# Optimization experiments

Hardware: AMD Instinct MI355X
Metric: run time of the kernel (lower is better)

Reference implementation:

```python
import jax, jax.numpy as jnp
import numpy as np
import math

N, H, D_MODEL = 2048, 16, 2048
D_K = D_MODEL // H
D_FF = 4 * D_MODEL
EPS = 1e-5


def _layernorm(x, alpha, beta):
    # torch: mean/var over dim=1 (=feature dim for 2D input), unbiased=False
    m = jnp.mean(x, axis=1, keepdims=True)
    v = jnp.var(x, axis=1, keepdims=True)
    return (x - m) / jnp.sqrt(v + EPS) * alpha + beta


def setup_inputs() -> dict:
    key = jax.random.key(0)
    ks = jax.random.split(key, 12)
    s = 0.02  # weight init scale
    return {
        "X": jax.random.normal(ks[0], (N, D_MODEL), jnp.float32),
        "Wq": jax.random.normal(ks[1], (H, D_MODEL, D_K), jnp.float32) * s,
        "bq": jax.random.normal(ks[2], (H, D_K), jnp.float32) * s,
        "Wk": jax.random.normal(ks[3], (H, D_MODEL, D_K), jnp.float32) * s,
        "bk": jax.random.normal(ks[4], (H, D_K), jnp.float32) * s,
        "Wv": jax.random.normal(ks[5], (H, D_MODEL, D_K), jnp.float32) * s,
        "bv": jax.random.normal(ks[6], (H, D_K), jnp.float32) * s,
        "alpha1": jnp.ones((N, D_MODEL), jnp.float32),
        "beta1": jnp.zeros((N, D_MODEL), jnp.float32),
        "W1": jax.random.normal(ks[7], (D_MODEL, D_FF), jnp.float32) * s,
        "b1": jax.random.normal(ks[8], (D_FF,), jnp.float32) * s,
        "W2": jax.random.normal(ks[9], (D_FF, D_MODEL), jnp.float32) * s,
        "b2": jax.random.normal(ks[10], (D_MODEL,), jnp.float32) * s,
        "alpha2": jnp.ones((N, D_MODEL), jnp.float32),
        "beta2": jnp.zeros((N, D_MODEL), jnp.float32),
    }


def reference(X, Wq, bq, Wk, bk, Wv, bv, alpha1, beta1, W1, b1, W2, b2, alpha2, beta2):
    # --- Multi-headed self-attention (h per-head linears fused as stacked weights) ---
    Q = jnp.einsum('nd,hdk->hnk', X, Wq) + bq[:, None, :]  # (H, N, D_K)
    K = jnp.einsum('nd,hdk->hnk', X, Wk) + bk[:, None, :]
    V = jnp.einsum('nd,hdk->hnk', X, Wv) + bv[:, None, :]
    scores = jnp.einsum('hnk,hmk->hnm', Q, K) / math.sqrt(D_K)  # (H, N, N)
    A = jax.nn.softmax(scores, axis=-1)  # softmax over keys (torch dim=1 of 2D)
    O = jnp.einsum('hnm,hmk->hnk', A, V)  # (H, N, D_K)
    attn = jnp.transpose(O, (1, 0, 2)).reshape(N, D_MODEL)  # concat heads on dim=1
    # --- Add & Norm 1 (dropout is identity at inference) ---
    h1 = _layernorm(X + attn, alpha1, beta1)
    # --- FFN ---
    ffn = jnp.maximum(h1 @ W1 + b1, 0.0) @ W2 + b2
    # --- Add & Norm 2 ---
    return _layernorm(h1 + ffn, alpha2, beta2)
```

## Files before the change

### kernel.cpp

```cpp
#include <hip/hip_runtime.h>
#include <hip/hip_bf16.h>

#define N_TOK 2048
#define DMODEL 2048
#define NH 16
#define DK 128
#define DFF 8192

typedef __attribute__((ext_vector_type(8))) short short8;
typedef __attribute__((ext_vector_type(4))) short s16x4;
typedef __attribute__((ext_vector_type(4))) float f32x4;

__device__ __forceinline__ short f2bf(float f) {
    unsigned int x = __builtin_bit_cast(unsigned int, f);
    unsigned int r = (x + 0x7fffu + ((x >> 16) & 1u)) >> 16;
    return (short)r;
}

__global__ __launch_bounds__(256) void cast_f32_bf16(const float* __restrict__ in,
                                                     short* __restrict__ out, int n8) {
    int i = blockIdx.x * 256 + threadIdx.x;
    if (i >= n8) return;
    const float4* p = (const float4*)in + (size_t)i * 2;
    float4 a = p[0], b = p[1];
    short8 o;
    o[0] = f2bf(a.x); o[1] = f2bf(a.y); o[2] = f2bf(a.z); o[3] = f2bf(a.w);
    o[4] = f2bf(b.x); o[5] = f2bf(b.y); o[6] = f2bf(b.z); o[7] = f2bf(b.w);
    *(short8*)(out + (size_t)i * 8) = o;
}

template <typename TIN>
__global__ __launch_bounds__(256) void transpose_cast(const TIN* __restrict__ in,
                                                      short* __restrict__ out,
                                                      int R, int C, long sIn, long sOut) {
    __shared__ float t[64][65];
    in  += (long)blockIdx.z * sIn;
    out += (long)blockIdx.z * sOut;
    int tx = threadIdx.x & 63, ty = threadIdx.x >> 6;
    long r0 = (long)blockIdx.y * 64, c0 = (long)blockIdx.x * 64;
    for (int i = 0; i < 16; i++) {
        int r = ty + i * 4;
        t[r][tx] = (float)in[(r0 + r) * (long)C + c0 + tx];
    }
    __syncthreads();
    for (int i = 0; i < 16; i++) {
        int r = ty + i * 4;
        out[(c0 + r) * (long)R + r0 + tx] = f2bf(t[tx][r]);
    }
}

__device__ __forceinline__ void gld_lds16(const void* g, void* l) {
    __builtin_amdgcn_global_load_lds(
        (const __attribute__((address_space(1))) void*)g,
        (__attribute__((address_space(3))) void*)l, 16, 0, 0);
}

#define VM8 asm volatile("s_waitcnt vmcnt(8)" ::: "memory")
#define VM0 asm volatile("s_waitcnt vmcnt(0)" ::: "memory")
#define VMNONE ((void)0)

#define PHASE(BUF, MH, NHI, RA, RBNH, STAGE_STMT, VMSTMT)                       \
  {                                                                             \
    if (RA) {                                                                   \
      _Pragma("unroll") for (int mp = 0; mp < 4; mp++)                          \
        _Pragma("unroll") for (int kk = 0; kk < 2; kk++) {                      \
          int rowA = wr * 128 + (MH) * 64 + mp * 16 + fr;                       \
          af[mp][kk] = *(const short8*)((const char*)lds + (BUF) * 65536 +      \
                         rowA * 128 + (((kk * 4 + fq) ^ (rowA & 7)) << 4));     \
        }                                                                       \
    }                                                                           \
    if ((RBNH) < 2) {                                                           \
      _Pragma("unroll") for (int np = 0; np < 2; np++)                          \
        _Pragma("unroll") for (int kk = 0; kk < 2; kk++) {                      \
          int rowB = wc * 64 + (RBNH) * 32 + np * 16 + fr;                      \
          bf[(RBNH) & 1][np][kk] =                                              \
              *(const short8*)((const char*)lds + (BUF) * 65536 + 32768 +       \
                  rowB * 128 + (((kk * 4 + fq) ^ (rowB & 7)) << 4));            \
        }                                                                       \
    }                                                                           \
    STAGE_STMT;                                                                 \
    __builtin_amdgcn_s_barrier();                                               \
    asm volatile("s_waitcnt lgkmcnt(0)" ::: "memory");                          \
    __builtin_amdgcn_sched_barrier(0);                                          \
    __builtin_amdgcn_s_setprio(1);                                              \
    _Pragma("unroll") for (int mp = 0; mp < 4; mp++)                            \
      _Pragma("unroll") for (int np = 0; np < 2; np++)                          \
        _Pragma("unroll") for (int kk = 0; kk < 2; kk++)                        \
          acc[(MH) * 4 + mp][(NHI) * 2 + np] =                                  \
              __builtin_amdgcn_mfma_f32_16x16x32_bf16(                          \
                  af[mp][kk], bf[NHI][np][kk], acc[(MH) * 4 + mp][(NHI) * 2 + np],\
                  0, 0, 0);                                                     \
    __builtin_amdgcn_s_setprio(0);                                              \
    VMSTMT;                                                                     \
    __builtin_amdgcn_sched_barrier(0);                                          \
    __builtin_amdgcn_s_barrier();                                               \
    __builtin_amdgcn_sched_barrier(0);                                          \
  }

template <int MODE>
__global__ __launch_bounds__(512, 2) void gemm256(const short* __restrict__ A,
                                                  const short* __restrict__ Bt,
                                                  void* __restrict__ Cv,
                                                  const float* __restrict__ b0,
                                                  const float* __restrict__ b1,
                                                  const float* __restrict__ b2,
                                                  int Ktot, int TM) {
    __shared__ short lds[65536];
    const int tid = threadIdx.x, lane = tid & 63, w = tid >> 6;
    const int T = gridDim.x, bid = blockIdx.x;
    const int vbid = (bid & 7) * (T >> 3) + (bid >> 3);
    const int mt = vbid % TM;
    const int rest = vbid / TM;
    int nt = rest, z = 0;
    if (MODE == 2) { nt = rest & 7; z = rest >> 3; }
    const long brow = (long)mt * 256, bcol = (long)nt * 256;
    const short* Ab = A + (MODE == 2 ? (long)z * 2048 : 0);
    const short* Bb = Bt + (MODE == 2 ? (long)z * 2048 : 0);

    auto stageA = [&](int kt, int buf, int mh) {
#pragma unroll
        for (int j = 0; j < 2; j++) {
            int row = mh * 64 + j * 128 + (tid >> 3);
            int g = (lane & 7) ^ (row & 7);
            gld_lds16((const char*)(Ab + (brow + row) * (long)Ktot + (long)kt * 64) + g * 16,
                      (char*)lds + buf * 65536 + mh * 8192 + j * 16384 + w * 1024 + lane * 16);
        }
    };
    auto stageB = [&](int kt, int buf, int nh) {
#pragma unroll
        for (int j = 0; j < 2; j++) {
            int s = 2 * j + (w >> 2);
            int rin = (w & 3) * 8 + (lane >> 3);
            int row = s * 64 + nh * 32 + rin;
            int g = (lane & 7) ^ (row & 7);
            gld_lds16((const char*)(Bb + (bcol + row) * (long)Ktot + (long)kt * 64) + g * 16,
                      (char*)lds + buf * 65536 + 32768 + j * 16384 + (w >> 2) * 8192 +
                          nh * 4096 + (w & 3) * 1024 + lane * 16);
        }
    };

    const int wr = w >> 2, wc = w & 3;
    const int fr = lane & 15, fq = lane >> 4;
    f32x4 acc[8][4] = {};
    short8 af[4][2], bf[2][2][2];

    stageA(0, 0, 0); stageB(0, 0, 0); stageB(0, 0, 1); stageA(0, 0, 1);
    stageA(1, 1, 0); stageB(1, 1, 0); stageB(1, 1, 1); stageA(1, 1, 1);
    VM8;
    __builtin_amdgcn_s_barrier();

    for (int i = 0; i < 15; i++) {
        const int kn = 2 * i + 2;
        PHASE(0, 0, 0, 1, 0, {}, VMNONE)
        PHASE(0, 0, 1, 0, 1, { stageA(kn, 0, 0); stageB(kn, 0, 0); }, VMNONE)
        PHASE(0, 1, 0, 1, 2, { stageB(kn, 0, 1); }, VMNONE)
        PHASE(0, 1, 1, 0, 2, { stageA(kn, 0, 1); }, VM8)
        PHASE(1, 0, 0, 1, 0, {}, VMNONE)
        PHASE(1, 0, 1, 0, 1, { stageA(kn + 1, 1, 0); stageB(kn + 1, 1, 0); }, VMNONE)
        PHASE(1, 1, 0, 1, 2, { stageB(kn + 1, 1, 1); }, VMNONE)
        PHASE(1, 1, 1, 0, 2, { stageA(kn + 1, 1, 1); }, VM8)
    }
    PHASE(0, 0, 0, 1, 0, {}, VMNONE)
    PHASE(0, 0, 1, 0, 1, {}, VMNONE)
    PHASE(0, 1, 0, 1, 2, {}, VMNONE)
    PHASE(0, 1, 1, 0, 2, {}, VM0)
    PHASE(1, 0, 0, 1, 0, {}, VMNONE)
    PHASE(1, 0, 1, 0, 1, {}, VMNONE)
    PHASE(1, 1, 0, 1, 2, {}, VMNONE)
    PHASE(1, 1, 1, 0, 2, {}, VMNONE)

    const long crow0 = brow + wr * 128, ccol0 = bcol + wc * 64;
#pragma unroll
    for (int n = 0; n < 4; n++) {
        const long col = ccol0 + (n >> 1) * 32 + (n & 1) * 16 + fr;
        float bval = 0.f;
        if (MODE == 0) {
            const float* bp = (col >> 11) == 0 ? b0 : (col >> 11) == 1 ? b1 : b2;
            bval = bp[col & 2047];
        } else if (MODE == 1) bval = b0[col];
#pragma unroll
        for (int m = 0; m < 8; m++) {
#pragma unroll
            for (int r = 0; r < 4; r++) {
                const long row = crow0 + (m >> 2) * 64 + (m & 3) * 16 + fq * 4 + r;
                float v = acc[m][n][r] + bval;
                if (MODE == 0) {
                    const long slab = col >> 7;
                    ((short*)Cv)[slab * (2048L * 128) + row * 128 + (col & 127)] = f2bf(v);
                } else if (MODE == 1) {
                    ((short*)Cv)[row * 8192 + col] = f2bf(fmaxf(v, 0.f));
                } else {
                    ((float*)Cv)[(long)z * (2048L * 2048) + row * 2048 + col] = v;
                }
            }
        }
    }
}

__global__ __launch_bounds__(512, 2) void attn_flash(const short* __restrict__ Q,
                                                     const short* __restrict__ Kc,
                                                     const short* __restrict__ VT,
                                                     float* __restrict__ O) {
    __shared__ short lds[32768];
    const int tid = threadIdx.x, lane = tid & 63, w = tid >> 6;
    const int bid = blockIdx.x;
    const int vid = (bid & 7) * 32 + (bid >> 3);
    const int h = vid >> 4, qt = vid & 15;
    const int fr = lane & 15, fq = lane >> 4;
    const long qbase = (long)qt * 128 + w * 16;
    const short* Qh = Q  + (long)h * N_TOK * DK;
    const short* Kh = Kc + (long)h * N_TOK * DK;
    const short* Vh = VT + (long)h * DK * N_TOK;
    short* Pw = lds + 24576 + w * 1024;

    short8 qf[4];
#pragma unroll
    for (int c = 0; c < 4; c++)
        qf[c] = *(const short8*)(Qh + (qbase + fr) * DK + c * 32 + fq * 8);

    float mrow = -1e30f, lrow = 0.f;
    f32x4 oacc[8] = {};
    const float C1 = 0.08838834764831845f * 1.4426950408889634f;

    int wr_off[4], rd_off[2];
#pragma unroll
    for (int jc = 0; jc < 4; jc++)
        wr_off[jc] = (fr * 64 + jc * 16 + fq * 4) ^ ((fr & 7) << 3);
#pragma unroll
    for (int kc = 0; kc < 2; kc++)
        rd_off[kc] = (fr * 64 + kc * 32 + fq * 8) ^ ((fr & 7) << 3);
    int colKb[4], colVb[2];
#pragma unroll
    for (int c = 0; c < 4; c++) colKb[c] = (c * 64 + fq * 16) ^ ((fr & 7) << 4);
#pragma unroll
    for (int kc = 0; kc < 2; kc++) colVb[kc] = (kc * 64 + fq * 16) ^ ((fr & 7) << 4);

    auto stageK = [&](int kvt, int buf) {
        const char* Kg = (const char*)(Kh + (long)kvt * 64 * DK);
        char* Kd = (char*)(lds + buf * 8192);
#pragma unroll
        for (int i = 0; i < 2; i++) {
            int a = (w * 2 + i) * 1024 + (lane << 4);
            int src = a ^ (((a >> 8) & 7) << 4);
            gld_lds16(Kg + src, Kd + (w * 2 + i) * 1024);
        }
    };
    auto stageV = [&](int kvt) {
        char* Vd = (char*)(lds + 16384);
#pragma unroll
        for (int i = 0; i < 2; i++) {
            int a = (w * 2 + i) * 1024 + (lane << 4);
            int row = a >> 7;
            int inner = (a & 127) ^ ((row & 7) << 4);
            const char* src = (const char*)Vh + ((long)row * N_TOK + (long)kvt * 64) * 2 + inner;
            gld_lds16(src, Vd + (w * 2 + i) * 1024);
        }
    };

    const int NT = N_TOK / 64;
    stageK(0, 0);
    __syncthreads();

    for (int t = 0; t < NT; t++) {
        const int cur = t & 1;
        stageV(t);
        if (t + 1 < NT) stageK(t + 1, cur ^ 1);

        const char* Kcb = (const char*)(lds + cur * 8192);
        f32x4 s[4] = {};
#pragma unroll
        for (int jc = 0; jc < 4; jc++) {
            const char* rb = Kcb + (jc * 16 + fr) * 256;
#pragma unroll
            for (int c = 0; c < 4; c++) {
                short8 kf = *(const short8*)(rb + colKb[c]);
                s[jc] = __builtin_amdgcn_mfma_f32_16x16x32_bf16(kf, qf[c], s[jc], 0, 0, 0);
            }
        }

        float tm = -1e30f;
#pragma unroll
        for (int jc = 0; jc < 4; jc++)
#pragma unroll
            for (int r = 0; r < 4; r++) tm = fmaxf(tm, s[jc][r]);
        tm = fmaxf(tm, __shfl_xor(tm, 16));
        tm = fmaxf(tm, __shfl_xor(tm, 32));
        float nm = fmaxf(mrow, tm);
        float resc = exp2f(C1 * (mrow - nm));
        mrow = nm;
        float sum = 0.f;
#pragma unroll
        for (int jc = 0; jc < 4; jc++)
#pragma unroll
            for (int r = 0; r < 4; r++) {
                float p = exp2f(C1 * (s[jc][r] - nm));
                s[jc][r] = p;
                sum += p;
            }
        sum += __shfl_xor(sum, 16);
        sum += __shfl_xor(sum, 32);
        lrow = lrow * resc + sum;
#pragma unroll
        for (int f = 0; f < 8; f++)
#pragma unroll
            for (int r = 0; r < 4; r++) oacc[f][r] *= resc;

#pragma unroll
        for (int jc = 0; jc < 4; jc++) {
            s16x4 pk;
            pk[0] = f2bf(s[jc][0]); pk[1] = f2bf(s[jc][1]);
            pk[2] = f2bf(s[jc][2]); pk[3] = f2bf(s[jc][3]);
            *(s16x4*)(Pw + wr_off[jc]) = pk;
        }
        short8 pa[2];
#pragma unroll
        for (int kc = 0; kc < 2; kc++)
            pa[kc] = *(const short8*)(Pw + rd_off[kc]);

        __syncthreads();

        const char* Vcb = (const char*)(lds + 16384);
#pragma unroll
        for (int f = 0; f < 8; f++) {
            const char* rb = Vcb + (f * 16 + fr) * 128;
#pragma unroll
            for (int kc = 0; kc < 2; kc++) {
                short8 vf = *(const short8*)(rb + colVb[kc]);
                oacc[f] = __builtin_amdgcn_mfma_f32_16x16x32_bf16(vf, pa[kc], oacc[f], 0, 0, 0);
            }
        }
        __syncthreads();
    }

    const float inv = 1.f / lrow;
    const long row = qbase + fr;
#pragma unroll
    for (int f = 0; f < 8; f++) {
        float4 o;
        o.x = oacc[f][0] * inv; o.y = oacc[f][1] * inv;
        o.z = oacc[f][2] * inv; o.w = oacc[f][3] * inv;
        *(float4*)(O + row * (long)DMODEL + h * DK + f * 16 + fq * 4) = o;
    }
}

template <bool WBF>
__global__ __launch_bounds__(256) void add_ln(const float* __restrict__ A,
                                              const float* __restrict__ B,
                                              const float* __restrict__ alpha,
                                              const float* __restrict__ beta,
                                              float* __restrict__ out,
                                              short* __restrict__ outbf) {
    const int row = blockIdx.x, t = threadIdx.x;
    const long base = (long)row * DMODEL;
    float4 va[2], vb[2];
    float s = 0.f, q = 0.f;
#pragma unroll
    for (int i = 0; i < 2; i++) {
        long off = base + (long)(t + i * 256) * 4;
        va[i] = *(const float4*)(A + off);
        vb[i] = *(const float4*)(B + off);
        float x0 = va[i].x + vb[i].x, x1 = va[i].y + vb[i].y;
        float x2 = va[i].z + vb[i].z, x3 = va[i].w + vb[i].w;
        s += x0 + x1 + x2 + x3;
        q += x0 * x0 + x1 * x1 + x2 * x2 + x3 * x3;
    }
#pragma unroll
    for (int o = 1; o < 64; o <<= 1) { s += __shfl_xor(s, o); q += __shfl_xor(q, o); }
    __shared__ float red[8];
    if ((t & 63) == 0) { red[t >> 6] = s; red[4 + (t >> 6)] = q; }
    __syncthreads();
    s = red[0] + red[1] + red[2] + red[3];
    q = red[4] + red[5] + red[6] + red[7];
    const float mean = s * (1.f / DMODEL);
    const float var = q * (1.f / DMODEL) - mean * mean;
    const float rstd = rsqrtf(var + 1e-5f);
#pragma unroll
    for (int i = 0; i < 2; i++) {
        long off = base + (long)(t + i * 256) * 4;
        float4 al = *(const float4*)(alpha + off);
        float4 be = *(const float4*)(beta + off);
        float x[4] = { va[i].x + vb[i].x, va[i].y + vb[i].y, va[i].z + vb[i].z, va[i].w + vb[i].w };
        float a[4] = { al.x, al.y, al.z, al.w };
        float b[4] = { be.x, be.y, be.z, be.w };
#pragma unroll
        for (int j = 0; j < 4; j++) {
            float o2 = (x[j] - mean) * rstd * a[j] + b[j];
            out[off + j] = o2;
            if (WBF) outbf[off + j] = f2bf(o2);
        }
    }
}

__global__ __launch_bounds__(256) void add_ln2_red(const float* __restrict__ H1,
                                                   const float* __restrict__ F4,
                                                   const float* __restrict__ b2,
                                                   const float* __restrict__ alpha,
                                                   const float* __restrict__ beta,
                                                   float* __restrict__ out) {
    const int row = blockIdx.x, t = threadIdx.x;
    const long base = (long)row * DMODEL;
    const long SL = (long)N_TOK * DMODEL;
    float x[8];
    float s = 0.f, q = 0.f;
#pragma unroll
    for (int i = 0; i < 2; i++) {
        long off = base + (long)(t + i * 256) * 4;
        int col = (t + i * 256) * 4;
        float4 a  = *(const float4*)(H1 + off);
        float4 f0 = *(const float4*)(F4 + off);
        float4 f1 = *(const float4*)(F4 + off + SL);
        float4 f2 = *(const float4*)(F4 + off + 2 * SL);
        float4 f3 = *(const float4*)(F4 + off + 3 * SL);
        float4 bb = *(const float4*)(b2 + col);
        x[i * 4 + 0] = a.x + f0.x + f1.x + f2.x + f3.x + bb.x;
        x[i * 4 + 1] = a.y + f0.y + f1.y + f2.y + f3.y + bb.y;
        x[i * 4 + 2] = a.z + f0.z + f1.z + f2.z + f3.z + bb.z;
        x[i * 4 + 3] = a.w + f0.w + f1.w + f2.w + f3.w + bb.w;
#pragma unroll
        for (int j = 0; j < 4; j++) { s += x[i * 4 + j]; q += x[i * 4 + j] * x[i * 4 + j]; }
    }
#pragma unroll
    for (int o = 1; o < 64; o <<= 1) { s += __shfl_xor(s, o); q += __shfl_xor(q, o); }
    __shared__ float red[8];
    if ((t & 63) == 0) { red[t >> 6] = s; red[4 + (t >> 6)] = q; }
    __syncthreads();
    s = red[0] + red[1] + red[2] + red[3];
    q = red[4] + red[5] + red[6] + red[7];
    const float mean = s * (1.f / DMODEL);
    const float var = q * (1.f / DMODEL) - mean * mean;
    const float rstd = rsqrtf(var + 1e-5f);
#pragma unroll
    for (int i = 0; i < 2; i++) {
        long off = base + (long)(t + i * 256) * 4;
        float4 al = *(const float4*)(alpha + off);
        float4 be = *(const float4*)(beta + off);
        float a[4] = { al.x, al.y, al.z, al.w };
        float b[4] = { be.x, be.y, be.z, be.w };
#pragma unroll
        for (int j = 0; j < 4; j++)
            out[off + j] = (x[i * 4 + j] - mean) * rstd * a[j] + b[j];
    }
}

extern "C" void kernel_launch(void* const* d_in, const int* in_sizes, int n_in,
                              void* d_out, int out_size, void* d_ws, size_t ws_size,
                              hipStream_t stream) {
    const float* X      = (const float*)d_in[0];
    const float* Wq     = (const float*)d_in[1];
    const float* bq     = (const float*)d_in[2];
    const float* Wk     = (const float*)d_in[3];
    const float* bk     = (const float*)d_in[4];
    const float* Wv     = (const float*)d_in[5];
    const float* bv     = (const float*)d_in[6];
    const float* alpha1 = (const float*)d_in[7];
    const float* beta1  = (const float*)d_in[8];
    const float* W1     = (const float*)d_in[9];
    const float* b1     = (const float*)d_in[10];
    const float* W2     = (const float*)d_in[11];
    const float* b2     = (const float*)d_in[12];
    const float* alpha2 = (const float*)d_in[13];
    const float* beta2  = (const float*)d_in[14];
    float* out = (float*)d_out;

    char* ws = (char*)d_ws;
    size_t off = 0;
    auto alloc = [&](size_t bytes) -> void* {
        void* p = ws + off;
        off += (bytes + 255) & ~(size_t)255;
        return p;
    };
    short* XBF   = (short*)alloc(2048UL * 2048 * 2);
    short* WQKVT = (short*)alloc(48UL * 128 * 2048 * 2);
    short* W1T   = (short*)alloc(8192UL * 2048 * 2);
    short* W2T   = (short*)alloc(2048UL * 8192 * 2);
    short* QKV   = (short*)alloc(48UL * 2048 * 128 * 2);
    short* VT    = (short*)alloc(16UL * 128 * 2048 * 2);
    float* ATTN  = (float*)alloc(2048UL * 2048 * 4);
    float* H1    = (float*)alloc(2048UL * 2048 * 4);
    short* H1BF  = (short*)alloc(2048UL * 2048 * 2);
    short* G     = (short*)alloc(2048UL * 8192 * 2);
    float* F4 = (float*)XBF;

    cast_f32_bf16<<<2048, 256, 0, stream>>>(X, XBF, 2048 * 2048 / 8);
    transpose_cast<float><<<dim3(2, 32, 16), 256, 0, stream>>>(Wq, WQKVT,                    2048, 128, 2048L * 128, 128L * 2048);
    transpose_cast<float><<<dim3(2, 32, 16), 256, 0, stream>>>(Wk, WQKVT + 16L * 128 * 2048, 2048, 128, 2048L * 128, 128L * 2048);
    transpose_cast<float><<<dim3(2, 32, 16), 256, 0, stream>>>(Wv, WQKVT + 32L * 128 * 2048, 2048, 128, 2048L * 128, 128L * 2048);
    transpose_cast<float><<<dim3(128, 32, 1), 256, 0, stream>>>(W1, W1T, 2048, 8192, 0, 0);
    transpose_cast<float><<<dim3(32, 128, 1), 256, 0, stream>>>(W2, W2T, 8192, 2048, 0, 0);

    gemm256<0><<<192, 512, 0, stream>>>(XBF, WQKVT, QKV, bq, bk, bv, 2048, 8);

    transpose_cast<__hip_bfloat16><<<dim3(2, 32, 16), 256, 0, stream>>>(
        (const __hip_bfloat16*)(QKV + 32L * 2048 * 128), VT, 2048, 128, 2048L * 128, 128L * 2048);

    attn_flash<<<256, 512, 0, stream>>>(QKV, QKV + 16L * 2048 * 128, VT, ATTN);

    add_ln<true><<<2048, 256, 0, stream>>>(X, ATTN, alpha1, beta1, H1, H1BF);

    gemm256<1><<<256, 512, 0, stream>>>(H1BF, W1T, G, b1, nullptr, nullptr, 2048, 8);
    gemm256<2><<<256, 512, 0, stream>>>(G, W2T, F4, nullptr, nullptr, nullptr, 8192, 8);

    add_ln2_red<<<2048, 256, 0, stream>>>(H1, F4, b2, alpha2, beta2, out);
}
```

Baseline: 378.8 us.

## Deepen attention K/V prefetch ring, vectorize transpose stores, store FFN split-K partials in bf16

The attention kernel replaces its double-buffered K plus single V buffer with a four-deep ring for both K and V. Loads are issued several tiles ahead and gated by vmcnt waits and a raw s_barrier, which drops one of the two __syncthreads per tile. The transpose-cast kernel now writes 8 bf16 values per 16-byte store instead of scalar shorts. The split-K FFN2 partial sums are stored as bf16 rather than fp32, roughly halving that round trip. The trade-offs are much larger LDS use in attention (about 144KB per block), which likely hurts occupancy under launch_bounds(512,2), and some precision loss in the partial sums.

```diff
diff --git a/kernel.cpp b/kernel.cpp
--- a/kernel.cpp
+++ b/kernel.cpp
@@ -15,6 +15,10 @@
     unsigned int x = __builtin_bit_cast(unsigned int, f);
     unsigned int r = (x + 0x7fffu + ((x >> 16) & 1u)) >> 16;
     return (short)r;
+}
+__device__ __forceinline__ float bf2f(short s) {
+    unsigned int u = ((unsigned int)(unsigned short)s) << 16;
+    return __builtin_bit_cast(float, u);
 }
 
 __global__ __launch_bounds__(256) void cast_f32_bf16(const float* __restrict__ in,
@@ -36,16 +40,22 @@
     __shared__ float t[64][65];
     in  += (long)blockIdx.z * sIn;
     out += (long)blockIdx.z * sOut;
-    int tx = threadIdx.x & 63, ty = threadIdx.x >> 6;
+    const int tid = threadIdx.x;
+    int tx = tid & 63, ty = tid >> 6;
     long r0 = (long)blockIdx.y * 64, c0 = (long)blockIdx.x * 64;
     for (int i = 0; i < 16; i++) {
         int r = ty + i * 4;
         t[r][tx] = (float)in[(r0 + r) * (long)C + c0 + tx];
     }
     __syncthreads();
-    for (int i = 0; i < 16; i++) {
-        int r = ty + i * 4;
-        out[(c0 + r) * (long)R + r0 + tx] = f2bf(t[tx][r]);
+#pragma unroll
+    for (int p = 0; p < 2; p++) {
+        int c = (tid >> 3) + p * 32;
+        int r8 = (tid & 7) * 8;
+        short8 v;
+#pragma unroll
+        for (int j = 0; j < 8; j++) v[j] = f2bf(t[r8 + j][c]);
+        *(short8*)(out + (c0 + c) * (long)R + r0 + r8) = v;
     }
 }
 
@@ -190,7 +200,7 @@
                 } else if (MODE == 1) {
                     ((short*)Cv)[row * 8192 + col] = f2bf(fmaxf(v, 0.f));
                 } else {
-                    ((float*)Cv)[(long)z * (2048L * 2048) + row * 2048 + col] = v;
+                    ((short*)Cv)[(long)z * (2048L * 2048) + row * 2048 + col] = f2bf(v);
                 }
             }
         }
@@ -201,7 +211,7 @@
                                                      const short* __restrict__ Kc,
                                                      const short* __restrict__ VT,
                                                      float* __restrict__ O) {
-    __shared__ short lds[32768];
+    __shared__ short lds[73728];
     const int tid = threadIdx.x, lane = tid & 63, w = tid >> 6;
     const int bid = blockIdx.x;
     const int vid = (bid & 7) * 32 + (bid >> 3);
@@ -211,7 +221,7 @@
     const short* Qh = Q  + (long)h * N_TOK * DK;
     const short* Kh = Kc + (long)h * N_TOK * DK;
     const short* Vh = VT + (long)h * DK * N_TOK;
-    short* Pw = lds + 24576 + w * 1024;
+    short* Pw = lds + 65536 + w * 1024;
 
     short8 qf[4];
 #pragma unroll
@@ -235,9 +245,10 @@
 #pragma unroll
     for (int kc = 0; kc < 2; kc++) colVb[kc] = (kc * 64 + fq * 16) ^ ((fr & 7) << 4);
 
-    auto stageK = [&](int kvt, int buf) {
+    auto stageK = [&](int kvt) {
+        const int buf = kvt & 3;
         const char* Kg = (const char*)(Kh + (long)kvt * 64 * DK);
-        char* Kd = (char*)(lds + buf * 8192);
+        char* Kd = (char*)lds + buf * 16384;
 #pragma unroll
         for (int i = 0; i < 2; i++) {
             int a = (w * 2 + i) * 1024 + (lane << 4);
@@ -246,7 +257,8 @@
         }
     };
     auto stageV = [&](int kvt) {
-        char* Vd = (char*)(lds + 16384);
+        const int buf = kvt & 3;
+        char* Vd = (char*)lds + 65536 + buf * 16384;
 #pragma unroll
         for (int i = 0; i < 2; i++) {
             int a = (w * 2 + i) * 1024 + (lane << 4);
@@ -258,15 +270,13 @@
     };
 
     const int NT = N_TOK / 64;
-    stageK(0, 0);
-    __syncthreads();
+    stageK(0); stageV(0); stageK(1); stageV(1); stageK(2); stageV(2); stageK(3);
+    asm volatile("s_waitcnt vmcnt(12)" ::: "memory");
+    __builtin_amdgcn_s_barrier();
+    __builtin_amdgcn_sched_barrier(0);
 
     for (int t = 0; t < NT; t++) {
-        const int cur = t & 1;
-        stageV(t);
-        if (t + 1 < NT) stageK(t + 1, cur ^ 1);
-
-        const char* Kcb = (const char*)(lds + cur * 8192);
+        const char* Kcb = (const char*)lds + (t & 3) * 16384;
         f32x4 s[4] = {};
 #pragma unroll
         for (int jc = 0; jc < 4; jc++) {
@@ -317,9 +327,13 @@
         for (int kc = 0; kc < 2; kc++)
             pa[kc] = *(const short8*)(Pw + rd_off[kc]);
 
-        __syncthreads();
-
-        const char* Vcb = (const char*)(lds + 16384);
+        if (t < NT - 4) asm volatile("s_waitcnt vmcnt(8)" ::: "memory");
+        else            asm volatile("s_waitcnt vmcnt(0)" ::: "memory");
+        __builtin_amdgcn_sched_barrier(0);
+        __builtin_amdgcn_s_barrier();
+        __builtin_amdgcn_sched_barrier(0);
+
+        const char* Vcb = (const char*)lds + 65536 + (t & 3) * 16384;
 #pragma unroll
         for (int f = 0; f < 8; f++) {
             const char* rb = Vcb + (f * 16 + fr) * 128;
@@ -329,7 +343,9 @@
                 oacc[f] = __builtin_amdgcn_mfma_f32_16x16x32_bf16(vf, pa[kc], oacc[f], 0, 0, 0);
             }
         }
-        __syncthreads();
+
+        if (t + 4 < NT) stageK(t + 4);
+        if (t + 3 < NT) stageV(t + 3);
     }
 
     const float inv = 1.f / lrow;
@@ -392,7 +408,7 @@
 }
 
 __global__ __launch_bounds__(256) void add_ln2_red(const float* __restrict__ H1,
-                                                   const float* __restrict__ F4,
+                                                   const short* __restrict__ F4,
                                                    const float* __restrict__ b2,
                                                    const float* __restrict__ alpha,
                                                    const float* __restrict__ beta,
@@ -407,17 +423,18 @@
         long off = base + (long)(t + i * 256) * 4;
         int col = (t + i * 256) * 4;
         float4 a  = *(const float4*)(H1 + off);
-        float4 f0 = *(const float4*)(F4 + off);
-        float4 f1 = *(const float4*)(F4 + off + SL);
-        float4 f2 = *(const float4*)(F4 + off + 2 * SL);
-        float4 f3 = *(const float4*)(F4 + off + 3 * SL);
+        s16x4 f0 = *(const s16x4*)(F4 + off);
+        s16x4 f1 = *(const s16x4*)(F4 + off + SL);
+        s16x4 f2 = *(const s16x4*)(F4 + off + 2 * SL);
+        s16x4 f3 = *(const s16x4*)(F4 + off + 3 * SL);
         float4 bb = *(const float4*)(b2 + col);
-        x[i * 4 + 0] = a.x + f0.x + f1.x + f2.x + f3.x + bb.x;
-        x[i * 4 + 1] = a.y + f0.y + f1.y + f2.y + f3.y + bb.y;
-        x[i * 4 + 2] = a.z + f0.z + f1.z + f2.z + f3.z + bb.z;
-        x[i * 4 + 3] = a.w + f0.w + f1.w + f2.w + f3.w + bb.w;
-#pragma unroll
-        for (int j = 0; j < 4; j++) { s += x[i * 4 + j]; q += x[i * 4 + j] * x[i * 4 + j]; }
+        float xa[4] = { a.x + bb.x, a.y + bb.y, a.z + bb.z, a.w + bb.w };
+#pragma unroll
+        for (int j = 0; j < 4; j++) {
+            float v = xa[j] + bf2f(f0[j]) + bf2f(f1[j]) + bf2f(f2[j]) + bf2f(f3[j]);
+            x[i * 4 + j] = v;
+            s += v; q += v * v;
+        }
     }
 #pragma unroll
     for (int o = 1; o < 64; o <<= 1) { s += __shfl_xor(s, o); q += __shfl_xor(q, o); }
@@ -479,7 +496,7 @@
     float* H1    = (float*)alloc(2048UL * 2048 * 4);
     short* H1BF  = (short*)alloc(2048UL * 2048 * 2);
     short* G     = (short*)alloc(2048UL * 8192 * 2);
-    float* F4 = (float*)XBF;
+    short* F4 = XBF;
 
     cast_f32_bf16<<<2048, 256, 0, stream>>>(X, XBF, 2048 * 2048 / 8);
     transpose_cast<float><<<dim3(2, 32, 16), 256, 0, stream>>>(Wq, WQKVT,                    2048, 128, 2048L * 128, 128L * 2048);
```

Result: no change. 371.7 us (-1.9%).
